# Kernel tuning notes

Hardware: AMD Instinct MI355X
Metric: run time of the kernel (lower is better)

The kernel has to match this reference:

```python
import jax, jax.numpy as jnp
import numpy as np

BITS = 4
MAXQ = (1 << BITS) - 1          # 15
PACK = 32 // BITS               # 8 values per int32
GROUP_SIZE = 128
IN_F, OUT_F = 4096, 11008


def setup_inputs() -> dict:
    key = jax.random.key(0)
    k1, k2, k3, k4, k5 = jax.random.split(key, 5)
    x = jax.random.normal(k1, (4, 2048, IN_F), dtype=jnp.float32)
    scales = jax.random.uniform(k2, (IN_F // GROUP_SIZE, OUT_F), dtype=jnp.float32) * 0.01
    bias = jax.random.normal(k3, (OUT_F,), dtype=jnp.float32)
    qweight = jax.random.randint(k4, (IN_F // PACK, OUT_F), 0, 2147483647, dtype=jnp.int32)
    qzeros = jax.random.randint(k5, (IN_F // GROUP_SIZE, OUT_F // PACK), 0, 2147483647, dtype=jnp.int32)
    return {"x": x, "scales": scales, "bias": bias, "qweight": qweight, "qzeros": qzeros}


def _dequant(qweight, qzeros, scales):
    shifts = (jnp.arange(PACK, dtype=jnp.int32) * BITS)
    # unpack along dim0: each int32 row holds PACK consecutive input rows
    w = ((qweight[:, None, :] >> shifts[None, :, None]) & MAXQ)  # [IN_F/PACK, PACK, OUT_F]
    w = w.reshape(IN_F, OUT_F).astype(scales.dtype)
    # unpack along dim1: each int32 col holds PACK consecutive output cols
    z = ((qzeros[:, :, None] >> shifts[None, None, :]) & MAXQ)   # [G, OUT_F/PACK, PACK]
    z = z.reshape(qzeros.shape[0], OUT_F).astype(scales.dtype)
    # per-group affine dequant: (w - zero) * scale
    weight = ((w.reshape(-1, GROUP_SIZE, OUT_F) - z[:, None, :]) * scales[:, None, :])
    return weight.reshape(IN_F, OUT_F)


def reference(x, scales, bias, qweight, qzeros):
    weight = _dequant(qweight, qzeros, scales).astype(x.dtype)
    out = jnp.matmul(x, weight)  # [B, S, OUT_F]
    return out + bias.astype(out.dtype)
```

## Files before the change

kernel.cpp:

```cpp
#include <hip/hip_runtime.h>
#include <hip/hip_bf16.h>
#include <stdint.h>

#define IN_F   4096
#define OUT_F  11008
#define M_TOT  8192
#define ZCOLS  (OUT_F / 8)
#define KK_ROWS (IN_F / 8)

#define BM 256
#define BN 256
#define BK 64
#define NT (IN_F / BK)
#define GRID_M (M_TOT / BM)
#define GRID_N (OUT_F / BN)
#define NWG (GRID_M * GRID_N)
#define CPX (NWG / 8)

typedef __attribute__((ext_vector_type(8))) short  bf16x8;
typedef __attribute__((ext_vector_type(8))) ushort ushort8;
typedef __attribute__((ext_vector_type(4))) float  f32x4;

__device__ __forceinline__ ushort f2bf(float f) {
    __hip_bfloat16 h = __float2bfloat16(f);
    return *reinterpret_cast<ushort*>(&h);
}

__global__ void convert_x(const float4* __restrict__ x, ushort8* __restrict__ xb) {
    size_t t = (size_t)blockIdx.x * 256 + threadIdx.x;
    float4 a = x[2 * t];
    float4 b = x[2 * t + 1];
    ushort8 o;
    o[0] = f2bf(a.x); o[1] = f2bf(a.y); o[2] = f2bf(a.z); o[3] = f2bf(a.w);
    o[4] = f2bf(b.x); o[5] = f2bf(b.y); o[6] = f2bf(b.z); o[7] = f2bf(b.w);
    xb[t] = o;
}

__global__ void dequant_w(const int* __restrict__ qw, const int* __restrict__ qz,
                          const float* __restrict__ sc, ushort* __restrict__ wt) {
    int t  = blockIdx.x * 256 + threadIdx.x;
    int n  = t >> 9;
    int kk = t & 511;
    int g  = kk >> 4;
    int w  = qw[kk * OUT_F + n];
    int z  = (qz[g * ZCOLS + (n >> 3)] >> ((n & 7) * 4)) & 15;
    float s = sc[g * OUT_F + n];
    ushort r[8];
#pragma unroll
    for (int i = 0; i < 8; ++i) {
        int q = (w >> (4 * i)) & 15;
        r[i] = f2bf((float)(q - z) * s);
    }
    ushort4* dst = (ushort4*)(wt + (size_t)n * IN_F + kk * 8);
    dst[0] = make_ushort4(r[0], r[1], r[2], r[3]);
    dst[1] = make_ushort4(r[4], r[5], r[6], r[7]);
}

__global__ __launch_bounds__(512, 2)
void gemm_bf16(const ushort* __restrict__ A, const ushort* __restrict__ Bt,
               const float* __restrict__ bias, float* __restrict__ C) {
    __shared__ ushort smem[8][8192];

    const int tid  = threadIdx.x;
    const int wave = tid >> 6;
    const int lane = tid & 63;

    const int bid = blockIdx.x;
    const int swz = (bid & 7) * CPX + (bid >> 3);
    const int bm0 = (swz / GRID_N) * BM;
    const int bn0 = (swz % GRID_N) * BN;

    const int wm = wave >> 2;
    const int wn = wave & 3;
    const int lm = lane & 15;
    const int lq = lane >> 4;

    const int sr   = lane >> 3;
    const int scol = 8 * ((lane & 7) ^ sr);

    const ushort* aSrc[2][2];
    const ushort* bSrc[2][2];
#pragma unroll
    for (int j = 0; j < 2; ++j) {
        const int r = wave * 16 + j * 8 + sr;
#pragma unroll
        for (int h = 0; h < 2; ++h) {
            aSrc[h][j] = A  + (size_t)(bm0 + ((r >> 6) << 7) + h * 64 + (r & 63)) * IN_F + scol;
            bSrc[h][j] = Bt + (size_t)(bn0 + ((r >> 5) << 6) + h * 32 + (r & 31)) * IN_F + scol;
        }
    }

    const int cswz0 = (lq * 8)      ^ ((lm & 7) << 3);
    const int cswz1 = (32 + lq * 8) ^ ((lm & 7) << 3);

    f32x4  acc[8][4] = {};
    bf16x8 af[4][2];
    bf16x8 bfv[2][2];

#define STAGE_A(buf, mh, kt) do {                                                        \
    _Pragma("unroll")                                                                    \
    for (int j_ = 0; j_ < 2; ++j_)                                                       \
        __builtin_amdgcn_global_load_lds(                                                \
            (const __attribute__((address_space(1))) void*)(aSrc[mh][j_] + (size_t)(kt) * BK), \
            (__attribute__((address_space(3))) void*)(&smem[(buf) * 4 + (mh)][(wave * 2 + j_) * 512]), \
            16, 0, 0);                                                                   \
} while (0)

#define STAGE_B(buf, nh, kt) do {                                                        \
    _Pragma("unroll")                                                                    \
    for (int j_ = 0; j_ < 2; ++j_)                                                       \
        __builtin_amdgcn_global_load_lds(                                                \
            (const __attribute__((address_space(1))) void*)(bSrc[nh][j_] + (size_t)(kt) * BK), \
            (__attribute__((address_space(3))) void*)(&smem[(buf) * 4 + 2 + (nh)][(wave * 2 + j_) * 512]), \
            16, 0, 0);                                                                   \
} while (0)

#define LDA(buf, mh) do {                                                                \
    const ushort* ab_ = &smem[(buf) * 4 + (mh)][wm * 4096 + lm * 64];                    \
    _Pragma("unroll")                                                                    \
    for (int i_ = 0; i_ < 4; ++i_) {                                                     \
        af[i_][0] = *(const bf16x8*)(ab_ + i_ * 1024 + cswz0);                           \
        af[i_][1] = *(const bf16x8*)(ab_ + i_ * 1024 + cswz1);                           \
    }                                                                                    \
} while (0)

#define LDB(buf, nh) do {                                                                \
    const ushort* bb_ = &smem[(buf) * 4 + 2 + (nh)][wn * 2048 + lm * 64];                \
    _Pragma("unroll")                                                                    \
    for (int j_ = 0; j_ < 2; ++j_) {                                                     \
        bfv[j_][0] = *(const bf16x8*)(bb_ + j_ * 1024 + cswz0);                          \
        bfv[j_][1] = *(const bf16x8*)(bb_ + j_ * 1024 + cswz1);                          \
    }                                                                                    \
} while (0)

#define MFMA_Q(mh, nh) do {                                                              \
    __builtin_amdgcn_s_setprio(1);                                                       \
    _Pragma("unroll")                                                                    \
    for (int i_ = 0; i_ < 4; ++i_)                                                       \
        _Pragma("unroll")                                                                \
        for (int j_ = 0; j_ < 2; ++j_)                                                   \
            _Pragma("unroll")                                                            \
            for (int k_ = 0; k_ < 2; ++k_)                                               \
                acc[(mh) * 4 + i_][(nh) * 2 + j_] = __builtin_amdgcn_mfma_f32_16x16x32_bf16( \
                    af[i_][k_], bfv[j_][k_], acc[(mh) * 4 + i_][(nh) * 2 + j_], 0, 0, 0); \
    __builtin_amdgcn_s_setprio(0);                                                       \
} while (0)

#define BAR()   asm volatile("s_barrier" ::: "memory")
#define LGKM0() asm volatile("s_waitcnt lgkmcnt(0)" ::: "memory")
#define VM(n)   asm volatile("s_waitcnt vmcnt(" #n ")" ::: "memory")

    STAGE_A(0, 0, 0);
    STAGE_B(0, 1, 0);
    STAGE_A(0, 1, 0);
    STAGE_B(0, 0, 0);
    STAGE_A(1, 0, 1);
    STAGE_B(1, 1, 1);
    STAGE_A(1, 1, 1);
    VM(6);
    BAR();

#pragma unroll 1
    for (int it = 0; it < NT / 2; ++it) {
        const int t1 = 2 * it + 1;
        int s2 = 2 * it + 2; if (s2 > NT - 1) s2 = NT - 1;
        int s3 = 2 * it + 3; if (s3 > NT - 1) s3 = NT - 1;

        LDA(0, 0); LDB(0, 0);
        STAGE_B(1, 0, t1);
        BAR(); LGKM0();
        MFMA_Q(0, 0);
        BAR();

        LDB(0, 1);
        STAGE_A(0, 0, s2);
        BAR(); LGKM0();
        MFMA_Q(0, 1);
        BAR();

        LDA(0, 1);
        STAGE_B(0, 1, s2);
        BAR(); LGKM0();
        MFMA_Q(1, 1);
        BAR();

        LDB(0, 0);
        STAGE_A(0, 1, s2);
        BAR(); LGKM0();
        MFMA_Q(1, 0);
        VM(6);
        BAR();

        LDA(1, 0); LDB(1, 0);
        STAGE_B(0, 0, s2);
        BAR(); LGKM0();
        MFMA_Q(0, 0);
        BAR();

        LDB(1, 1);
        STAGE_A(1, 0, s3);
        BAR(); LGKM0();
        MFMA_Q(0, 1);
        BAR();

        LDA(1, 1);
        STAGE_B(1, 1, s3);
        BAR(); LGKM0();
        MFMA_Q(1, 1);
        BAR();

        LDB(1, 0);
        STAGE_A(1, 1, s3);
        BAR(); LGKM0();
        MFMA_Q(1, 0);
        VM(6);
        BAR();
    }

    VM(0);

    const int cm0 = bm0 + wm * 128 + lq * 4;
    const int cn0 = bn0 + wn * 64 + lm;
#pragma unroll
    for (int nt2 = 0; nt2 < 4; ++nt2) {
        const int n = cn0 + nt2 * 16;
        const float bv = bias[n];
#pragma unroll
        for (int mt = 0; mt < 8; ++mt) {
            float* out = C + (size_t)(cm0 + mt * 16) * OUT_F + n;
#pragma unroll
            for (int r = 0; r < 4; ++r)
                out[(size_t)r * OUT_F] = acc[mt][nt2][r] + bv;
        }
    }

#undef STAGE_A
#undef STAGE_B
#undef LDA
#undef LDB
#undef MFMA_Q
#undef BAR
#undef LGKM0
#undef VM
}

extern "C" void kernel_launch(void* const* d_in, const int* in_sizes, int n_in,
                              void* d_out, int out_size, void* d_ws, size_t ws_size,
                              hipStream_t stream) {
    const float* x       = (const float*)d_in[0];
    const float* scales  = (const float*)d_in[1];
    const float* bias    = (const float*)d_in[2];
    const int*   qweight = (const int*)d_in[3];
    const int*   qzeros  = (const int*)d_in[4];
    float* out = (float*)d_out;

    ushort* xb = (ushort*)d_ws;
    ushort* wt = (ushort*)((char*)d_ws + (size_t)M_TOT * IN_F * 2);

    convert_x<<<(M_TOT * IN_F / 8) / 256, 256, 0, stream>>>((const float4*)x, (ushort8*)xb);
    dequant_w<<<(OUT_F * KK_ROWS) / 256, 256, 0, stream>>>(qweight, qzeros, scales, wt);
    gemm_bf16<<<NWG, 512, 0, stream>>>(xb, wt, bias, out);
}
```

Measured before the change: 1.127 ms.

## Switch GEMM to 32x32x16 MFMA and transpose dequant output through LDS

The GEMM inner loop moves from 16x16x32 bf16 MFMA tiles to 32x32x16 tiles, changing the fragment layout, the LDS read offsets, the accumulator shape and the epilogue store mapping. Fewer, larger MFMAs per wave need fewer LDS fragment reads for the same work. The dequant kernel now stages a 64x64 tile in swizzled shared memory so writes to the transposed weight are coalesced 16-byte stores instead of strided ones. The cost is more accumulator registers per instruction and a new fragment mapping that must match the existing swizzle.

```diff
diff --git a/kernel.cpp b/kernel.cpp
--- a/kernel.cpp
+++ b/kernel.cpp
@@ -17,9 +17,9 @@
 #define NWG (GRID_M * GRID_N)
 #define CPX (NWG / 8)
 
-typedef __attribute__((ext_vector_type(8))) short  bf16x8;
-typedef __attribute__((ext_vector_type(8))) ushort ushort8;
-typedef __attribute__((ext_vector_type(4))) float  f32x4;
+typedef __attribute__((ext_vector_type(8)))  short  bf16x8;
+typedef __attribute__((ext_vector_type(8)))  ushort ushort8;
+typedef __attribute__((ext_vector_type(16))) float  f32x16;
 
 __device__ __forceinline__ ushort f2bf(float f) {
     __hip_bfloat16 h = __float2bfloat16(f);
@@ -36,24 +36,48 @@
     xb[t] = o;
 }
 
-__global__ void dequant_w(const int* __restrict__ qw, const int* __restrict__ qz,
-                          const float* __restrict__ sc, ushort* __restrict__ wt) {
-    int t  = blockIdx.x * 256 + threadIdx.x;
-    int n  = t >> 9;
-    int kk = t & 511;
-    int g  = kk >> 4;
-    int w  = qw[kk * OUT_F + n];
-    int z  = (qz[g * ZCOLS + (n >> 3)] >> ((n & 7) * 4)) & 15;
-    float s = sc[g * OUT_F + n];
-    ushort r[8];
-#pragma unroll
-    for (int i = 0; i < 8; ++i) {
-        int q = (w >> (4 * i)) & 15;
-        r[i] = f2bf((float)(q - z) * s);
-    }
-    ushort4* dst = (ushort4*)(wt + (size_t)n * IN_F + kk * 8);
-    dst[0] = make_ushort4(r[0], r[1], r[2], r[3]);
-    dst[1] = make_ushort4(r[4], r[5], r[6], r[7]);
+__global__ __launch_bounds__(256)
+void dequant_w(const int* __restrict__ qw, const int* __restrict__ qz,
+               const float* __restrict__ sc, ushort* __restrict__ wt) {
+    __shared__ ushort tile[64 * 512];
+
+    const int bid = blockIdx.x;
+    const int n0  = (bid % (OUT_F / 64)) * 64;
+    const int kk0 = (bid / (OUT_F / 64)) * 64;
+    const int tid = threadIdx.x;
+    const int nl  = tid & 63;
+    const int kr  = tid >> 6;
+
+    const int ng  = n0 + nl;
+    const int zsh = (ng & 7) * 4;
+    const int zc  = ng >> 3;
+
+#pragma unroll
+    for (int p = 0; p < 16; ++p) {
+        const int kk  = p * 4 + kr;
+        const int gkk = kk0 + kk;
+        const int g   = gkk >> 4;
+        const int w   = qw[gkk * OUT_F + ng];
+        const int z   = (qz[g * ZCOLS + zc] >> zsh) & 15;
+        const float s = sc[g * OUT_F + ng];
+        ushort8 r;
+#pragma unroll
+        for (int i = 0; i < 8; ++i) {
+            int q = (w >> (4 * i)) & 15;
+            r[i] = f2bf((float)(q - z) * s);
+        }
+        *(ushort8*)&tile[nl * 512 + ((kk * 8) ^ (nl << 3 & 511))] = r;
+    }
+    __syncthreads();
+
+    const int c   = tid & 63;
+    const int nr4 = tid >> 6;
+#pragma unroll
+    for (int p = 0; p < 16; ++p) {
+        const int nr = p * 4 + nr4;
+        ushort8 v = *(const ushort8*)&tile[nr * 512 + ((c * 8) ^ (nr << 3 & 511))];
+        *(ushort8*)&wt[(size_t)(n0 + nr) * IN_F + kk0 * 8 + c * 8] = v;
+    }
 }
 
 __global__ __launch_bounds__(512, 2)
@@ -72,8 +96,8 @@
 
     const int wm = wave >> 2;
     const int wn = wave & 3;
-    const int lm = lane & 15;
-    const int lq = lane >> 4;
+    const int la = lane & 31;
+    const int lh = lane >> 5;
 
     const int sr   = lane >> 3;
     const int scol = 8 * ((lane & 7) ^ sr);
@@ -90,12 +114,15 @@
         }
     }
 
-    const int cswz0 = (lq * 8)      ^ ((lm & 7) << 3);
-    const int cswz1 = (32 + lq * 8) ^ ((lm & 7) << 3);
-
-    f32x4  acc[8][4] = {};
-    bf16x8 af[4][2];
-    bf16x8 bfv[2][2];
+    const int sw8 = (la & 7) << 3;
+    int cof[4];
+#pragma unroll
+    for (int ks = 0; ks < 4; ++ks)
+        cof[ks] = (ks * 16 + lh * 8) ^ sw8;
+
+    f32x16 acc[4][2] = {};
+    bf16x8 af[2][4];
+    bf16x8 bfv[4];
 
 #define STAGE_A(buf, mh, kt) do {                                                        \
     _Pragma("unroll")                                                                    \
@@ -116,33 +143,29 @@
 } while (0)
 
 #define LDA(buf, mh) do {                                                                \
-    const ushort* ab_ = &smem[(buf) * 4 + (mh)][wm * 4096 + lm * 64];                    \
-    _Pragma("unroll")                                                                    \
-    for (int i_ = 0; i_ < 4; ++i_) {                                                     \
-        af[i_][0] = *(const bf16x8*)(ab_ + i_ * 1024 + cswz0);                           \
-        af[i_][1] = *(const bf16x8*)(ab_ + i_ * 1024 + cswz1);                           \
-    }                                                                                    \
+    const ushort* ab_ = &smem[(buf) * 4 + (mh)][(wm * 64 + la) * 64];                    \
+    _Pragma("unroll")                                                                    \
+    for (int i_ = 0; i_ < 2; ++i_)                                                       \
+        _Pragma("unroll")                                                                \
+        for (int ks_ = 0; ks_ < 4; ++ks_)                                                \
+            af[i_][ks_] = *(const bf16x8*)(ab_ + i_ * 2048 + cof[ks_]);                  \
 } while (0)
 
 #define LDB(buf, nh) do {                                                                \
-    const ushort* bb_ = &smem[(buf) * 4 + 2 + (nh)][wn * 2048 + lm * 64];                \
-    _Pragma("unroll")                                                                    \
-    for (int j_ = 0; j_ < 2; ++j_) {                                                     \
-        bfv[j_][0] = *(const bf16x8*)(bb_ + j_ * 1024 + cswz0);                          \
-        bfv[j_][1] = *(const bf16x8*)(bb_ + j_ * 1024 + cswz1);                          \
-    }                                                                                    \
+    const ushort* bb_ = &smem[(buf) * 4 + 2 + (nh)][(wn * 32 + la) * 64];                \
+    _Pragma("unroll")                                                                    \
+    for (int ks_ = 0; ks_ < 4; ++ks_)                                                    \
+        bfv[ks_] = *(const bf16x8*)(bb_ + cof[ks_]);                                     \
 } while (0)
 
 #define MFMA_Q(mh, nh) do {                                                              \
     __builtin_amdgcn_s_setprio(1);                                                       \
     _Pragma("unroll")                                                                    \
-    for (int i_ = 0; i_ < 4; ++i_)                                                       \
+    for (int i_ = 0; i_ < 2; ++i_)                                                       \
         _Pragma("unroll")                                                                \
-        for (int j_ = 0; j_ < 2; ++j_)                                                   \
-            _Pragma("unroll")                                                            \
-            for (int k_ = 0; k_ < 2; ++k_)                                               \
-                acc[(mh) * 4 + i_][(nh) * 2 + j_] = __builtin_amdgcn_mfma_f32_16x16x32_bf16( \
-                    af[i_][k_], bfv[j_][k_], acc[(mh) * 4 + i_][(nh) * 2 + j_], 0, 0, 0); \
+        for (int ks_ = 0; ks_ < 4; ++ks_)                                                \
+            acc[(mh) * 2 + i_][nh] = __builtin_amdgcn_mfma_f32_32x32x16_bf16(            \
+                af[i_][ks_], bfv[ks_], acc[(mh) * 2 + i_][nh], 0, 0, 0);                 \
     __builtin_amdgcn_s_setprio(0);                                                       \
 } while (0)
 
@@ -219,18 +242,20 @@
 
     VM(0);
 
-    const int cm0 = bm0 + wm * 128 + lq * 4;
-    const int cn0 = bn0 + wn * 64 + lm;
-#pragma unroll
-    for (int nt2 = 0; nt2 < 4; ++nt2) {
-        const int n = cn0 + nt2 * 16;
+#pragma unroll
+    for (int j = 0; j < 2; ++j) {
+        const int n = bn0 + wn * 64 + j * 32 + la;
         const float bv = bias[n];
 #pragma unroll
-        for (int mt = 0; mt < 8; ++mt) {
-            float* out = C + (size_t)(cm0 + mt * 16) * OUT_F + n;
-#pragma unroll
-            for (int r = 0; r < 4; ++r)
-                out[(size_t)r * OUT_F] = acc[mt][nt2][r] + bv;
+        for (int i = 0; i < 4; ++i) {
+            const int rowb = bm0 + wm * 128 + i * 32 + lh * 4;
+#pragma unroll
+            for (int rg = 0; rg < 4; ++rg) {
+                float* out = C + (size_t)(rowb + rg * 8) * OUT_F + n;
+#pragma unroll
+                for (int r = 0; r < 4; ++r)
+                    out[(size_t)r * OUT_F] = acc[i][j][rg * 4 + r] + bv;
+            }
         }
     }
 
@@ -258,6 +283,6 @@
     ushort* wt = (ushort*)((char*)d_ws + (size_t)M_TOT * IN_F * 2);
 
     convert_x<<<(M_TOT * IN_F / 8) / 256, 256, 0, stream>>>((const float4*)x, (ushort8*)xb);
-    dequant_w<<<(OUT_F * KK_ROWS) / 256, 256, 0, stream>>>(qweight, qzeros, scales, wt);
+    dequant_w<<<(OUT_F / 64) * (KK_ROWS / 64), 256, 0, stream>>>(qweight, qzeros, scales, wt);
     gemm_bf16<<<NWG, 512, 0, stream>>>(xb, wt, bias, out);
 }
```

New measurement: 1.183 ms. 4.9% more time.

## Coalesce dequant writes via LDS transpose tile and hoist B fragment loads

Applied to the files above, without the earlier changes.

The weight dequant kernel now processes a 64x64 tile per block, staging converted values in swizzled shared memory so that global stores to the transposed bf16 weight are contiguous along K instead of strided by IN_F. The GEMM loads both B n-halves into registers once per k-tile instead of reloading them before each MFMA quarter, cutting LDS read traffic. The cost is 64KB of LDS per dequant block and 32 extra VGPRs in the GEMM, which may pressure occupancy or cause spills.

```diff
diff --git a/kernel.cpp b/kernel.cpp
--- a/kernel.cpp
+++ b/kernel.cpp
@@ -36,24 +36,48 @@
     xb[t] = o;
 }
 
-__global__ void dequant_w(const int* __restrict__ qw, const int* __restrict__ qz,
-                          const float* __restrict__ sc, ushort* __restrict__ wt) {
-    int t  = blockIdx.x * 256 + threadIdx.x;
-    int n  = t >> 9;
-    int kk = t & 511;
-    int g  = kk >> 4;
-    int w  = qw[kk * OUT_F + n];
-    int z  = (qz[g * ZCOLS + (n >> 3)] >> ((n & 7) * 4)) & 15;
-    float s = sc[g * OUT_F + n];
-    ushort r[8];
-#pragma unroll
-    for (int i = 0; i < 8; ++i) {
-        int q = (w >> (4 * i)) & 15;
-        r[i] = f2bf((float)(q - z) * s);
-    }
-    ushort4* dst = (ushort4*)(wt + (size_t)n * IN_F + kk * 8);
-    dst[0] = make_ushort4(r[0], r[1], r[2], r[3]);
-    dst[1] = make_ushort4(r[4], r[5], r[6], r[7]);
+__global__ __launch_bounds__(256)
+void dequant_w(const int* __restrict__ qw, const int* __restrict__ qz,
+               const float* __restrict__ sc, ushort* __restrict__ wt) {
+    __shared__ ushort tile[64 * 512];
+
+    const int bid = blockIdx.x;
+    const int n0  = (bid % (OUT_F / 64)) * 64;
+    const int kk0 = (bid / (OUT_F / 64)) * 64;
+    const int tid = threadIdx.x;
+    const int nl  = tid & 63;
+    const int kr  = tid >> 6;
+
+    const int ng  = n0 + nl;
+    const int zsh = (ng & 7) * 4;
+    const int zc  = ng >> 3;
+
+#pragma unroll
+    for (int p = 0; p < 16; ++p) {
+        const int kk  = p * 4 + kr;
+        const int gkk = kk0 + kk;
+        const int g   = gkk >> 4;
+        const int w   = qw[gkk * OUT_F + ng];
+        const int z   = (qz[g * ZCOLS + zc] >> zsh) & 15;
+        const float s = sc[g * OUT_F + ng];
+        ushort8 r;
+#pragma unroll
+        for (int i = 0; i < 8; ++i) {
+            int q = (w >> (4 * i)) & 15;
+            r[i] = f2bf((float)(q - z) * s);
+        }
+        *(ushort8*)&tile[nl * 512 + ((kk * 8) ^ (nl << 3 & 511))] = r;
+    }
+    __syncthreads();
+
+    const int c   = tid & 63;
+    const int nr4 = tid >> 6;
+#pragma unroll
+    for (int p = 0; p < 16; ++p) {
+        const int nr = p * 4 + nr4;
+        ushort8 v = *(const ushort8*)&tile[nr * 512 + ((c * 8) ^ (nr << 3 & 511))];
+        *(ushort8*)&wt[(size_t)(n0 + nr) * IN_F + kk0 * 8 + c * 8] = v;
+    }
 }
 
 __global__ __launch_bounds__(512, 2)
@@ -95,7 +119,7 @@
 
     f32x4  acc[8][4] = {};
     bf16x8 af[4][2];
-    bf16x8 bfv[2][2];
+    bf16x8 ball[2][2][2];
 
 #define STAGE_A(buf, mh, kt) do {                                                        \
     _Pragma("unroll")                                                                    \
@@ -124,12 +148,15 @@
     }                                                                                    \
 } while (0)
 
-#define LDB(buf, nh) do {                                                                \
-    const ushort* bb_ = &smem[(buf) * 4 + 2 + (nh)][wn * 2048 + lm * 64];                \
-    _Pragma("unroll")                                                                    \
-    for (int j_ = 0; j_ < 2; ++j_) {                                                     \
-        bfv[j_][0] = *(const bf16x8*)(bb_ + j_ * 1024 + cswz0);                          \
-        bfv[j_][1] = *(const bf16x8*)(bb_ + j_ * 1024 + cswz1);                          \
+#define LDB2(buf) do {                                                                   \
+    _Pragma("unroll")                                                                    \
+    for (int nh_ = 0; nh_ < 2; ++nh_) {                                                  \
+        const ushort* bb_ = &smem[(buf) * 4 + 2 + nh_][wn * 2048 + lm * 64];             \
+        _Pragma("unroll")                                                                \
+        for (int j_ = 0; j_ < 2; ++j_) {                                                 \
+            ball[nh_][j_][0] = *(const bf16x8*)(bb_ + j_ * 1024 + cswz0);                \
+            ball[nh_][j_][1] = *(const bf16x8*)(bb_ + j_ * 1024 + cswz1);                \
+        }                                                                                \
     }                                                                                    \
 } while (0)
 
@@ -142,7 +169,7 @@
             _Pragma("unroll")                                                            \
             for (int k_ = 0; k_ < 2; ++k_)                                               \
                 acc[(mh) * 4 + i_][(nh) * 2 + j_] = __builtin_amdgcn_mfma_f32_16x16x32_bf16( \
-                    af[i_][k_], bfv[j_][k_], acc[(mh) * 4 + i_][(nh) * 2 + j_], 0, 0, 0); \
+                    af[i_][k_], ball[nh][j_][k_], acc[(mh) * 4 + i_][(nh) * 2 + j_], 0, 0, 0); \
     __builtin_amdgcn_s_setprio(0);                                                       \
 } while (0)
 
@@ -166,13 +193,12 @@
         int s2 = 2 * it + 2; if (s2 > NT - 1) s2 = NT - 1;
         int s3 = 2 * it + 3; if (s3 > NT - 1) s3 = NT - 1;
 
-        LDA(0, 0); LDB(0, 0);
+        LDA(0, 0); LDB2(0);
         STAGE_B(1, 0, t1);
         BAR(); LGKM0();
         MFMA_Q(0, 0);
         BAR();
 
-        LDB(0, 1);
         STAGE_A(0, 0, s2);
         BAR(); LGKM0();
         MFMA_Q(0, 1);
@@ -184,20 +210,18 @@
         MFMA_Q(1, 1);
         BAR();
 
-        LDB(0, 0);
         STAGE_A(0, 1, s2);
         BAR(); LGKM0();
         MFMA_Q(1, 0);
         VM(6);
         BAR();
 
-        LDA(1, 0); LDB(1, 0);
+        LDA(1, 0); LDB2(1);
         STAGE_B(0, 0, s2);
         BAR(); LGKM0();
         MFMA_Q(0, 0);
         BAR();
 
-        LDB(1, 1);
         STAGE_A(1, 0, s3);
         BAR(); LGKM0();
         MFMA_Q(0, 1);
@@ -209,7 +233,6 @@
         MFMA_Q(1, 1);
         BAR();
 
-        LDB(1, 0);
         STAGE_A(1, 1, s3);
         BAR(); LGKM0();
         MFMA_Q(1, 0);
@@ -237,7 +260,7 @@
 #undef STAGE_A
 #undef STAGE_B
 #undef LDA
-#undef LDB
+#undef LDB2
 #undef MFMA_Q
 #undef BAR
 #undef LGKM0
@@ -258,6 +281,6 @@
     ushort* wt = (ushort*)((char*)d_ws + (size_t)M_TOT * IN_F * 2);
 
     convert_x<<<(M_TOT * IN_F / 8) / 256, 256, 0, stream>>>((const float4*)x, (ushort8*)xb);
-    dequant_w<<<(OUT_F * KK_ROWS) / 256, 256, 0, stream>>>(qweight, qzeros, scales, wt);
+    dequant_w<<<(OUT_F / 64) * (KK_ROWS / 64), 256, 0, stream>>>(qweight, qzeros, scales, wt);
     gemm_bf16<<<NWG, 512, 0, stream>>>(xb, wt, bias, out);
 }
```

After: 1.074 ms. 1.05x faster.
